# Optimization experiments

Hardware: AMD Instinct MI355X
Metric: run time of the kernel (lower is better)

Reference implementation:

```python
import jax, jax.numpy as jnp
import numpy as np

B, S, D = 4, 2048, 1024
E, F = 8, 4096


def setup_inputs() -> dict:
    key = jax.random.key(0)
    ks = jax.random.split(key, 5)
    x = jax.random.normal(ks[0], (B, S, D), dtype=jnp.float32)
    switch_w = jax.random.normal(ks[1], (D, E), dtype=jnp.float32) * (D ** -0.5)
    switch_b = jnp.zeros((E,), dtype=jnp.float32)
    w1 = jax.random.normal(ks[2], (E, D, F), dtype=jnp.float32) * (D ** -0.5)
    b1 = jnp.zeros((E, F), dtype=jnp.float32)
    w2 = jax.random.normal(ks[3], (E, F, D), dtype=jnp.float32) * (F ** -0.5)
    b2 = jnp.zeros((E, D), dtype=jnp.float32)
    return {"x": x, "switch_w": switch_w, "switch_b": switch_b,
            "w1": w1, "b1": b1, "w2": w2, "b2": b2}


def reference(x, switch_w, switch_b, w1, b1, w2, b2):
    b, s, d = x.shape
    t = x.reshape(-1, d)                                  # [T, D] tokens
    logits = t @ switch_w + switch_b                      # [T, E]
    route_prob = jax.nn.softmax(logits, axis=-1)
    route_prob_max = jnp.max(route_prob, axis=-1)         # [T]
    routes = jnp.argmax(route_prob, axis=-1)              # [T] top-1 expert

    out = jnp.zeros_like(t)
    n_experts = w1.shape[0]
    for e in range(n_experts):                            # small fixed expert loop
        h = jax.nn.gelu(t @ w1[e] + b1[e])                # [T, F]
        y = h @ w2[e] + b2[e]                             # [T, D]
        mask = (routes == e)[:, None]
        out = jnp.where(mask, y, out)                     # scatter-combine by route

    out = out * route_prob_max[:, None]                   # is_scale_prob=True
    return out.reshape(b, s, d)
```

## Files before the change

kernel.cpp:

```cpp
#include <hip/hip_runtime.h>
#include <hip/hip_bf16.h>
#include <math.h>

#define T_TOK 8192
#define DIM   1024
#define NEXP  8
#define FF    4096
#define BM    256
#define BN    256
#define BK    64
#define TPAD  (T_TOK + NEXP * BM)
#define NCBLK 32
#define MT    (TPAD / BM)
#define NG1   640
#define NG2   160
#define NT2   4096

typedef __attribute__((ext_vector_type(4))) float  f32x4;
typedef __attribute__((ext_vector_type(8))) __bf16 bf16x8;

__global__ __launch_bounds__(256) void router_kernel(const float* __restrict__ x,
                              const float* __restrict__ sw, const float* __restrict__ sb,
                              int* __restrict__ route, float* __restrict__ scale,
                              __hip_bfloat16* __restrict__ xb)
{
    int wave = threadIdx.x >> 6, lane = threadIdx.x & 63;
    int t = blockIdx.x * 4 + wave;
    const float* xr = x + (size_t)t * DIM + lane * 16;

    float xv[16];
#pragma unroll
    for (int i = 0; i < 4; ++i)
        *(float4*)&xv[i * 4] = *(const float4*)(xr + i * 4);

    bf16x8 u0, u1;
#pragma unroll
    for (int i = 0; i < 8; ++i) { u0[i] = (__bf16)xv[i]; u1[i] = (__bf16)xv[i + 8]; }
    __hip_bfloat16* xo = xb + (size_t)t * DIM + lane * 16;
    *(bf16x8*)xo = u0;
    *(bf16x8*)(xo + 8) = u1;

    double acc[NEXP];
#pragma unroll
    for (int e = 0; e < NEXP; ++e) acc[e] = 0.0;
    const float* swp = sw + lane * 16 * NEXP;
#pragma unroll
    for (int j = 0; j < 16; ++j) {
        float4 s0 = *(const float4*)(swp + j * 8);
        float4 s1 = *(const float4*)(swp + j * 8 + 4);
        double xd = (double)xv[j];
        acc[0] += xd * (double)s0.x; acc[1] += xd * (double)s0.y;
        acc[2] += xd * (double)s0.z; acc[3] += xd * (double)s0.w;
        acc[4] += xd * (double)s1.x; acc[5] += xd * (double)s1.y;
        acc[6] += xd * (double)s1.z; acc[7] += xd * (double)s1.w;
    }
#pragma unroll
    for (int e = 0; e < NEXP; ++e) {
        double v = acc[e];
        for (int off = 32; off; off >>= 1) v += __shfl_down(v, off);
        acc[e] = v;
    }
    if (lane == 0) {
        double m = -1e300; int am = 0;
#pragma unroll
        for (int e = 0; e < NEXP; ++e) {
            double v = acc[e] + (double)sb[e];
            acc[e] = v;
            if (v > m) { m = v; am = e; }
        }
        double s = 0.0;
#pragma unroll
        for (int e = 0; e < NEXP; ++e) s += exp(acc[e] - m);
        route[t] = am;
        scale[t] = (float)(1.0 / s);
    }
}

__global__ __launch_bounds__(256) void count_kernel(const int* __restrict__ route,
                                                    int* __restrict__ bc)
{
    __shared__ int c[NEXP];
    if (threadIdx.x < NEXP) c[threadIdx.x] = 0;
    __syncthreads();
    int t = blockIdx.x * 256 + threadIdx.x;
    atomicAdd(&c[route[t]], 1);
    __syncthreads();
    if (threadIdx.x < NEXP) bc[blockIdx.x * NEXP + threadIdx.x] = c[threadIdx.x];
}

__global__ __launch_bounds__(64) void offsets_kernel(const int* __restrict__ bc,
                                                     int* __restrict__ offPad,
                                                     int* __restrict__ base)
{
    int l = threadIdx.x & 31;
    int cnt[NEXP], pre[NEXP], tot[NEXP];
#pragma unroll
    for (int e = 0; e < NEXP; ++e) cnt[e] = bc[l * NEXP + e];
#pragma unroll
    for (int e = 0; e < NEXP; ++e) {
        int v = cnt[e];
#pragma unroll
        for (int d = 1; d < 32; d <<= 1) {
            int u = __shfl_up(v, d, 32);
            if (l >= d) v += u;
        }
        pre[e] = v - cnt[e];
        tot[e] = __shfl(v, 31, 32);
    }
    int o = 0, off[NEXP];
#pragma unroll
    for (int e = 0; e < NEXP; ++e) {
        off[e] = o;
        o += ((tot[e] + BM - 1) / BM) * BM;
    }
    if (l == 0) {
#pragma unroll
        for (int e = 0; e < NEXP; ++e) offPad[e] = off[e];
        offPad[NEXP] = o;
    }
#pragma unroll
    for (int e = 0; e < NEXP; ++e) base[l * NEXP + e] = off[e] + pre[e];
}

__global__ __launch_bounds__(256) void scatter_kernel(const int* __restrict__ route,
                                                      const int* __restrict__ base,
                                                      int* __restrict__ perm)
{
    __shared__ int cur[NEXP];
    if (threadIdx.x < NEXP) cur[threadIdx.x] = base[blockIdx.x * NEXP + threadIdx.x];
    __syncthreads();
    int t = blockIdx.x * 256 + threadIdx.x;
    int pos = atomicAdd(&cur[route[t]], 1);
    perm[pos] = t;
}

__global__ __launch_bounds__(256) void transpose_cvt64(const float* __restrict__ src,
                                                       __hip_bfloat16* __restrict__ dst,
                                                       int R, int C)
{
    __shared__ float tile[64][65];
    size_t bofs = (size_t)blockIdx.z * (size_t)R * (size_t)C;
    int c0 = blockIdx.x * 64, r0 = blockIdx.y * 64;
    int t = threadIdx.x;
    int tx = t & 15, ty = t >> 4;
#pragma unroll
    for (int i = 0; i < 4; ++i) {
        int r = ty + i * 16;
        float4 v = *(const float4*)(src + bofs + (size_t)(r0 + r) * C + c0 + tx * 4);
        tile[r][tx * 4 + 0] = v.x; tile[r][tx * 4 + 1] = v.y;
        tile[r][tx * 4 + 2] = v.z; tile[r][tx * 4 + 3] = v.w;
    }
    __syncthreads();
    int sx = t & 7, sy = t >> 3;
#pragma unroll
    for (int i = 0; i < 2; ++i) {
        int oc = sy + i * 32;
        bf16x8 u;
#pragma unroll
        for (int j = 0; j < 8; ++j)
            u[j] = (__bf16)tile[sx * 8 + j][oc];
        *(bf16x8*)(dst + bofs + (size_t)(c0 + oc) * R + r0 + sx * 8) = u;
    }
}

#define STAGE_A(b, h, t) do { \
    __builtin_amdgcn_global_load_lds((const __attribute__((address_space(1))) void*)(aSrc[h][0] + (size_t)(t) * 64), \
        (__attribute__((address_space(3))) void*)(ldsA + (b) * 32768 + (h) * 16384 + wid * 1024), 16, 0, 0); \
    __builtin_amdgcn_global_load_lds((const __attribute__((address_space(1))) void*)(aSrc[h][1] + (size_t)(t) * 64), \
        (__attribute__((address_space(3))) void*)(ldsA + (b) * 32768 + (h) * 16384 + (wid + 8) * 1024), 16, 0, 0); \
} while (0)

#define STAGE_B(b, h, t) do { \
    __builtin_amdgcn_global_load_lds((const __attribute__((address_space(1))) void*)(bSrc[h][0] + (size_t)(t) * 64), \
        (__attribute__((address_space(3))) void*)(ldsB + (b) * 32768 + (h) * 16384 + wid * 1024), 16, 0, 0); \
    __builtin_amdgcn_global_load_lds((const __attribute__((address_space(1))) void*)(bSrc[h][1] + (size_t)(t) * 64), \
        (__attribute__((address_space(3))) void*)(ldsB + (b) * 32768 + (h) * 16384 + (wid + 8) * 1024), 16, 0, 0); \
} while (0)

#define VMW asm volatile("s_waitcnt vmcnt(4)" ::: "memory")

#define PHASE(B_, MH, KS, LOADB, STAGEX, VMX) do { \
    __builtin_amdgcn_sched_barrier(0); \
    bf16x8 af[4]; \
    _Pragma("unroll") \
    for (int i_ = 0; i_ < 4; ++i_) \
        af[i_] = *(const bf16x8*)(aRd + (B_) * 32768 + ((MH) * 4 + i_) * 2048 + kOff[KS]); \
    if (LOADB) { \
        _Pragma("unroll") \
        for (int n_ = 0; n_ < 4; ++n_) \
            bfr[KS][n_] = *(const bf16x8*)(bRd + (B_) * 32768 + n_ * 2048 + kOff[KS]); \
    } \
    STAGEX; \
    __builtin_amdgcn_s_barrier(); \
    asm volatile("s_waitcnt lgkmcnt(0)" ::: "memory"); \
    __builtin_amdgcn_sched_barrier(0); \
    __builtin_amdgcn_s_setprio(1); \
    _Pragma("unroll") \
    for (int i_ = 0; i_ < 4; ++i_) \
        _Pragma("unroll") \
        for (int n_ = 0; n_ < 4; ++n_) \
            acc[(MH) * 4 + i_][n_] = __builtin_amdgcn_mfma_f32_16x16x32_bf16(af[i_], bfr[KS][n_], acc[(MH) * 4 + i_][n_], 0, 0, 0); \
    __builtin_amdgcn_s_setprio(0); \
    VMX; \
    __builtin_amdgcn_s_barrier(); \
} while (0)

template<int MODE>
__global__ __launch_bounds__(512, 2) void moe_gemm8(
    const __hip_bfloat16* __restrict__ A,
    const __hip_bfloat16* __restrict__ Bw,
    const float* __restrict__ bias,
    const int* __restrict__ offPad,
    const int* __restrict__ perm,
    const float* __restrict__ scale,
    __hip_bfloat16* __restrict__ Hout,
    float* __restrict__ Out,
    const float* __restrict__ w2src,
    __hip_bfloat16* __restrict__ w2tdst,
    const int K, const int N)
{
    __shared__ char lds[131072];
    const int tid = threadIdx.x;
    const int bid = blockIdx.x;
    const int NG  = MODE ? NG2 : NG1;

    if (MODE == 0 && bid >= NG1) {
        const int j    = bid - NG1;
        const int t2   = tid & 255;
        const int half = tid >> 8;
        const int tile_id = j * 2 + half;
        const int cx = tile_id & 15;
        const int ry = (tile_id >> 4) & 63;
        const int ez = tile_id >> 10;
        float (*tl)[65] = (float (*)[65])(lds + half * 17408);
        const float* src = w2src + (size_t)ez * FF * DIM;
        __hip_bfloat16* dst = w2tdst + (size_t)ez * DIM * FF;
        const int c0 = cx * 64, r0 = ry * 64;
        const int tx = t2 & 15, ty = t2 >> 4;
#pragma unroll
        for (int i = 0; i < 4; ++i) {
            int r = ty + i * 16;
            float4 v = *(const float4*)(src + (size_t)(r0 + r) * DIM + c0 + tx * 4);
            tl[r][tx * 4 + 0] = v.x; tl[r][tx * 4 + 1] = v.y;
            tl[r][tx * 4 + 2] = v.z; tl[r][tx * 4 + 3] = v.w;
        }
        __syncthreads();
        const int sx = t2 & 7, sy = t2 >> 3;
#pragma unroll
        for (int i = 0; i < 2; ++i) {
            int oc = sy + i * 32;
            bf16x8 u;
#pragma unroll
            for (int jj = 0; jj < 8; ++jj)
                u[jj] = (__bf16)tl[sx * 8 + jj][oc];
            *(bf16x8*)(dst + (size_t)(c0 + oc) * FF + r0 + sx * 8) = u;
        }
        return;
    }

    const int swz = (bid & 7) * (NG >> 3) + (bid >> 3);
    const int mt  = swz % MT;
    const int nt  = swz / MT;
    const int m0  = mt * BM;
    if (m0 >= offPad[NEXP]) return;
    int e = 0;
    while (offPad[e + 1] <= m0) ++e;

    char* ldsA = lds;
    char* ldsB = lds + 65536;

    const int lane = tid & 63;
    const int wid  = tid >> 6;
    const int wr   = wid >> 2;
    const int wc   = wid & 3;
    const int g    = lane >> 4, rl = lane & 15;

    const __hip_bfloat16* Bp = Bw + (size_t)e * (size_t)N * (size_t)K;

    const int l3 = lane >> 3;
    const int colOff = ((lane & 7) ^ l3) * 8;
    const __hip_bfloat16* aSrc[2][2];
    const __hip_bfloat16* bSrc[2][2];
#pragma unroll
    for (int h = 0; h < 2; ++h)
#pragma unroll
        for (int j = 0; j < 2; ++j) {
            int r = (wid + j * 8) * 8 + l3;
            int arow = m0 + h * 128 + r;
            size_t ar;
            if (MODE == 0) { int tk = perm[arow]; ar = (size_t)(tk < 0 ? 0 : tk); }
            else           { ar = (size_t)arow; }
            aSrc[h][j] = A + ar * (size_t)K + colOff;
            bSrc[h][j] = Bp + (size_t)(nt * BN + h * 128 + r) * (size_t)K + colOff;
        }

    const char* aRd = ldsA + wr * 16384 + rl * 128;
    const char* bRd = ldsB + (wc >> 1) * 16384 + (wc & 1) * 8192 + rl * 128;
    int kOff[2];
    kOff[0] = ((0 * 4 + g) ^ (rl & 7)) * 16;
    kOff[1] = ((1 * 4 + g) ^ (rl & 7)) * 16;

    f32x4 acc[8][4];
#pragma unroll
    for (int i = 0; i < 8; ++i)
#pragma unroll
        for (int n = 0; n < 4; ++n) acc[i][n] = (f32x4)0.0f;
    bf16x8 bfr[2][4];

    const int ntiles = K >> 6;

    STAGE_A(0, 0, 0); STAGE_A(0, 1, 0);
    STAGE_B(0, 0, 0); STAGE_B(0, 1, 0);
    STAGE_B(1, 0, 1); STAGE_B(1, 1, 1);
    asm volatile("s_waitcnt vmcnt(4)" ::: "memory");
    __builtin_amdgcn_s_barrier();

    for (int it = 0; it < (ntiles >> 1); ++it) {
        const int t1 = 2 * it + 1;
        const int t2 = 2 * it + 2 < ntiles ? 2 * it + 2 : ntiles - 1;
        const int t3 = 2 * it + 3 < ntiles ? 2 * it + 3 : ntiles - 1;
        PHASE(0, 0, 0, true,  STAGE_A(1, 0, t1), );
        PHASE(0, 0, 1, true,  STAGE_A(1, 1, t1), );
        PHASE(0, 1, 0, false, STAGE_B(0, 0, t2), );
        PHASE(0, 1, 1, false, STAGE_B(0, 1, t2), VMW);
        PHASE(1, 0, 0, true,  STAGE_A(0, 0, t2), );
        PHASE(1, 0, 1, true,  STAGE_A(0, 1, t2), );
        PHASE(1, 1, 0, false, STAGE_B(1, 0, t3), );
        PHASE(1, 1, 1, false, STAGE_B(1, 1, t3), VMW);
    }
    asm volatile("s_waitcnt vmcnt(0)" ::: "memory");

    const int colBase = nt * BN + wc * 64;
    const int rowBase = m0 + wr * 128;
    float bcol[4];
#pragma unroll
    for (int n = 0; n < 4; ++n) bcol[n] = bias[(size_t)e * N + colBase + n * 16 + rl];

    if (MODE == 0) {
#pragma unroll
        for (int m = 0; m < 8; ++m) {
#pragma unroll
            for (int r = 0; r < 4; ++r) {
                int row = rowBase + m * 16 + g * 4 + r;
                __hip_bfloat16* hrow = Hout + (size_t)row * N + colBase;
#pragma unroll
                for (int n = 0; n < 4; ++n) {
                    float v = acc[m][n][r] + bcol[n];
                    float u = -1.5957691216057308f * (v + 0.044715f * v * v * v);
                    float gel = v / (1.f + __expf(u));
                    hrow[n * 16 + rl] = __float2bfloat16(gel);
                }
            }
        }
    } else {
#pragma unroll
        for (int m = 0; m < 8; ++m) {
#pragma unroll
            for (int r = 0; r < 4; ++r) {
                int row = rowBase + m * 16 + g * 4 + r;
                int tk = perm[row];
                if (tk >= 0) {
                    float sc = scale[tk];
                    float* orow = Out + (size_t)tk * N + colBase;
#pragma unroll
                    for (int n = 0; n < 4; ++n)
                        orow[n * 16 + rl] = (acc[m][n][r] + bcol[n]) * sc;
                }
            }
        }
    }
}

extern "C" void kernel_launch(void* const* d_in, const int* in_sizes, int n_in,
                              void* d_out, int out_size, void* d_ws, size_t ws_size,
                              hipStream_t stream)
{
    const float* x  = (const float*)d_in[0];
    const float* sw = (const float*)d_in[1];
    const float* sb = (const float*)d_in[2];
    const float* w1 = (const float*)d_in[3];
    const float* b1 = (const float*)d_in[4];
    const float* w2 = (const float*)d_in[5];
    const float* b2 = (const float*)d_in[6];
    float* out = (float*)d_out;
    char* ws = (char*)d_ws;

    int*   bc     = (int*)(ws + 1024);
    int*   base   = (int*)(ws + 2048);
    int*   offPad = (int*)(ws + 3072);
    int*   route  = (int*)(ws + 4096);
    float* scale  = (float*)(ws + 36864);
    int*   perm   = (int*)(ws + 69632);

    const size_t offXb   = 131072;
    const size_t szXb    = (size_t)T_TOK * DIM * 2;
    const size_t offW1   = offXb + szXb;
    const size_t szW     = (size_t)NEXP * DIM * FF * 2;
    const size_t offW2   = offW1 + szW;
    const size_t szH     = (size_t)TPAD * FF * 2;
    const size_t offHF   = offW2 + szW;
    const size_t needF   = offHF + szH;

    const bool fuseT = ws_size >= needF;

    __hip_bfloat16* xb  = (__hip_bfloat16*)(ws + offXb);
    __hip_bfloat16* w1t = (__hip_bfloat16*)(ws + offW1);
    __hip_bfloat16* w2t = (__hip_bfloat16*)(ws + (fuseT ? offW2 : offW1));
    __hip_bfloat16* h   = (__hip_bfloat16*)(ws + (fuseT ? offHF : offW2));

    hipMemsetAsync(perm, 0xFF, TPAD * 4, stream);

    router_kernel<<<T_TOK / 4, 256, 0, stream>>>(x, sw, sb, route, scale, xb);
    count_kernel<<<NCBLK, 256, 0, stream>>>(route, bc);
    offsets_kernel<<<1, 64, 0, stream>>>(bc, offPad, base);
    scatter_kernel<<<NCBLK, 256, 0, stream>>>(route, base, perm);

    transpose_cvt64<<<dim3(FF / 64, DIM / 64, NEXP), 256, 0, stream>>>(w1, w1t, DIM, FF);

    if (fuseT) {
        moe_gemm8<0><<<NG1 + NT2, 512, 0, stream>>>(
            xb, w1t, b1, offPad, perm, scale, h, nullptr, w2, w2t, DIM, FF);
        moe_gemm8<1><<<NG2, 512, 0, stream>>>(
            h, w2t, b2, offPad, perm, scale, nullptr, out, nullptr, nullptr, FF, DIM);
    } else {
        moe_gemm8<0><<<NG1, 512, 0, stream>>>(
            xb, w1t, b1, offPad, perm, scale, h, nullptr, nullptr, nullptr, DIM, FF);
        transpose_cvt64<<<dim3(DIM / 64, FF / 64, NEXP), 256, 0, stream>>>(w2, w2t, FF, DIM);
        moe_gemm8<1><<<NG2, 512, 0, stream>>>(
            h, w2t, b2, offPad, perm, scale, nullptr, out, nullptr, nullptr, FF, DIM);
    }
}
```

Before: 315.6 us.

## Shrink MoE GEMM tiles to 128x256 with BK=32 triple-buffered pipeline

```diff
diff --git a/kernel.cpp b/kernel.cpp
--- a/kernel.cpp
+++ b/kernel.cpp
@@ -6,14 +6,13 @@
 #define DIM   1024
 #define NEXP  8
 #define FF    4096
-#define BM    256
+#define BM    128
 #define BN    256
-#define BK    64
 #define TPAD  (T_TOK + NEXP * BM)
 #define NCBLK 32
 #define MT    (TPAD / BM)
-#define NG1   640
-#define NG2   160
+#define NG1   (16 * MT)
+#define NG2   (4 * MT)
 #define NT2   4096
 
 typedef __attribute__((ext_vector_type(4))) float  f32x4;
@@ -163,50 +162,44 @@
     }
 }
 
-#define STAGE_A(b, h, t) do { \
-    __builtin_amdgcn_global_load_lds((const __attribute__((address_space(1))) void*)(aSrc[h][0] + (size_t)(t) * 64), \
-        (__attribute__((address_space(3))) void*)(ldsA + (b) * 32768 + (h) * 16384 + wid * 1024), 16, 0, 0); \
-    __builtin_amdgcn_global_load_lds((const __attribute__((address_space(1))) void*)(aSrc[h][1] + (size_t)(t) * 64), \
-        (__attribute__((address_space(3))) void*)(ldsA + (b) * 32768 + (h) * 16384 + (wid + 8) * 1024), 16, 0, 0); \
+#define GL2LDS(g, l) __builtin_amdgcn_global_load_lds( \
+    (const __attribute__((address_space(1))) void*)(g), \
+    (__attribute__((address_space(3))) void*)(l), 16, 0, 0)
+
+#define STG(TS, BUFS) do { \
+    const int ts_ = (TS) < NT ? (TS) : NT - 1; \
+    const size_t ko_ = (size_t)ts_ * 32; \
+    GL2LDS(aSrc + ko_, lds + (BUFS) * 24576 + dstA); \
+    GL2LDS(bSrc0 + ko_, lds + (BUFS) * 24576 + 8192 + dstA); \
+    GL2LDS(bSrc1 + ko_, lds + (BUFS) * 24576 + 16384 + dstA); \
 } while (0)
 
-#define STAGE_B(b, h, t) do { \
-    __builtin_amdgcn_global_load_lds((const __attribute__((address_space(1))) void*)(bSrc[h][0] + (size_t)(t) * 64), \
-        (__attribute__((address_space(3))) void*)(ldsB + (b) * 32768 + (h) * 16384 + wid * 1024), 16, 0, 0); \
-    __builtin_amdgcn_global_load_lds((const __attribute__((address_space(1))) void*)(bSrc[h][1] + (size_t)(t) * 64), \
-        (__attribute__((address_space(3))) void*)(ldsB + (b) * 32768 + (h) * 16384 + (wid + 8) * 1024), 16, 0, 0); \
-} while (0)
-
-#define VMW asm volatile("s_waitcnt vmcnt(4)" ::: "memory")
-
-#define PHASE(B_, MH, KS, LOADB, STAGEX, VMX) do { \
+#define PH(BUFR, TS, BUFS) do { \
     __builtin_amdgcn_sched_barrier(0); \
-    bf16x8 af[4]; \
+    bf16x8 af[4], bf[4]; \
     _Pragma("unroll") \
     for (int i_ = 0; i_ < 4; ++i_) \
-        af[i_] = *(const bf16x8*)(aRd + (B_) * 32768 + ((MH) * 4 + i_) * 2048 + kOff[KS]); \
-    if (LOADB) { \
-        _Pragma("unroll") \
-        for (int n_ = 0; n_ < 4; ++n_) \
-            bfr[KS][n_] = *(const bf16x8*)(bRd + (B_) * 32768 + n_ * 2048 + kOff[KS]); \
-    } \
-    STAGEX; \
+        af[i_] = *(const bf16x8*)(lds + (BUFR) * 24576 + aOff + i_ * 1024); \
+    _Pragma("unroll") \
+    for (int n_ = 0; n_ < 4; ++n_) \
+        bf[n_] = *(const bf16x8*)(lds + (BUFR) * 24576 + bOff + n_ * 1024); \
+    STG(TS, BUFS); \
     __builtin_amdgcn_s_barrier(); \
     asm volatile("s_waitcnt lgkmcnt(0)" ::: "memory"); \
     __builtin_amdgcn_sched_barrier(0); \
     __builtin_amdgcn_s_setprio(1); \
     _Pragma("unroll") \
-    for (int i_ = 0; i_ < 4; ++i_) \
+    for (int m_ = 0; m_ < 4; ++m_) \
         _Pragma("unroll") \
         for (int n_ = 0; n_ < 4; ++n_) \
-            acc[(MH) * 4 + i_][n_] = __builtin_amdgcn_mfma_f32_16x16x32_bf16(af[i_], bfr[KS][n_], acc[(MH) * 4 + i_][n_], 0, 0, 0); \
+            acc[m_][n_] = __builtin_amdgcn_mfma_f32_16x16x32_bf16(af[m_], bf[n_], acc[m_][n_], 0, 0, 0); \
     __builtin_amdgcn_s_setprio(0); \
-    VMX; \
+    asm volatile("s_waitcnt vmcnt(3)" ::: "memory"); \
     __builtin_amdgcn_s_barrier(); \
 } while (0)
 
 template<int MODE>
-__global__ __launch_bounds__(512, 2) void moe_gemm8(
+__global__ __launch_bounds__(512, 4) void moe_gemm32(
     const __hip_bfloat16* __restrict__ A,
     const __hip_bfloat16* __restrict__ Bw,
     const float* __restrict__ bias,
@@ -216,13 +209,16 @@
     __hip_bfloat16* __restrict__ Hout,
     float* __restrict__ Out,
     const float* __restrict__ w2src,
-    __hip_bfloat16* __restrict__ w2tdst,
-    const int K, const int N)
-{
-    __shared__ char lds[131072];
+    __hip_bfloat16* __restrict__ w2tdst)
+{
+    constexpr int K  = MODE ? FF : DIM;
+    constexpr int N  = MODE ? DIM : FF;
+    constexpr int NT = K / 32;
+    constexpr int NG = MODE ? NG2 : NG1;
+
+    __shared__ char lds[73728];
     const int tid = threadIdx.x;
     const int bid = blockIdx.x;
-    const int NG  = MODE ? NG2 : NG1;
 
     if (MODE == 0 && bid >= NG1) {
         const int j    = bid - NG1;
@@ -266,9 +262,6 @@
     int e = 0;
     while (offPad[e + 1] <= m0) ++e;
 
-    char* ldsA = lds;
-    char* ldsB = lds + 65536;
-
     const int lane = tid & 63;
     const int wid  = tid >> 6;
     const int wr   = wid >> 2;
@@ -277,68 +270,50 @@
 
     const __hip_bfloat16* Bp = Bw + (size_t)e * (size_t)N * (size_t)K;
 
-    const int l3 = lane >> 3;
-    const int colOff = ((lane & 7) ^ l3) * 8;
-    const __hip_bfloat16* aSrc[2][2];
-    const __hip_bfloat16* bSrc[2][2];
-#pragma unroll
-    for (int h = 0; h < 2; ++h)
-#pragma unroll
-        for (int j = 0; j < 2; ++j) {
-            int r = (wid + j * 8) * 8 + l3;
-            int arow = m0 + h * 128 + r;
-            size_t ar;
-            if (MODE == 0) { int tk = perm[arow]; ar = (size_t)(tk < 0 ? 0 : tk); }
-            else           { ar = (size_t)arow; }
-            aSrc[h][j] = A + ar * (size_t)K + colOff;
-            bSrc[h][j] = Bp + (size_t)(nt * BN + h * 128 + r) * (size_t)K + colOff;
-        }
-
-    const char* aRd = ldsA + wr * 16384 + rl * 128;
-    const char* bRd = ldsB + (wc >> 1) * 16384 + (wc & 1) * 8192 + rl * 128;
-    int kOff[2];
-    kOff[0] = ((0 * 4 + g) ^ (rl & 7)) * 16;
-    kOff[1] = ((1 * 4 + g) ^ (rl & 7)) * 16;
-
-    f32x4 acc[8][4];
-#pragma unroll
-    for (int i = 0; i < 8; ++i)
+    const int colElem = (((lane & 3) ^ ((lane >> 2) & 3) ^ ((lane >> 4) & 1))) * 8;
+    const int srow = wid * 16 + (lane >> 2);
+    size_t ar;
+    if (MODE == 0) { int tk = perm[m0 + srow]; ar = (size_t)(tk < 0 ? 0 : tk); }
+    else           { ar = (size_t)(m0 + srow); }
+    const __hip_bfloat16* aSrc  = A  + ar * (size_t)K + colElem;
+    const __hip_bfloat16* bSrc0 = Bp + (size_t)(nt * BN + srow) * (size_t)K + colElem;
+    const __hip_bfloat16* bSrc1 = bSrc0 + (size_t)128 * K;
+    const int dstA = wid * 1024 + lane * 16;
+
+    const int kOff = ((g ^ (rl & 3) ^ ((rl >> 2) & 1))) * 16;
+    const int aOff = wr * 4096 + rl * 64 + kOff;
+    const int bOff = 8192 + wc * 4096 + rl * 64 + kOff;
+
+    f32x4 acc[4][4];
+#pragma unroll
+    for (int i = 0; i < 4; ++i)
 #pragma unroll
         for (int n = 0; n < 4; ++n) acc[i][n] = (f32x4)0.0f;
-    bf16x8 bfr[2][4];
-
-    const int ntiles = K >> 6;
-
-    STAGE_A(0, 0, 0); STAGE_A(0, 1, 0);
-    STAGE_B(0, 0, 0); STAGE_B(0, 1, 0);
-    STAGE_B(1, 0, 1); STAGE_B(1, 1, 1);
-    asm volatile("s_waitcnt vmcnt(4)" ::: "memory");
+
+    STG(0, 0); STG(1, 1);
+    asm volatile("s_waitcnt vmcnt(3)" ::: "memory");
     __builtin_amdgcn_s_barrier();
 
-    for (int it = 0; it < (ntiles >> 1); ++it) {
-        const int t1 = 2 * it + 1;
-        const int t2 = 2 * it + 2 < ntiles ? 2 * it + 2 : ntiles - 1;
-        const int t3 = 2 * it + 3 < ntiles ? 2 * it + 3 : ntiles - 1;
-        PHASE(0, 0, 0, true,  STAGE_A(1, 0, t1), );
-        PHASE(0, 0, 1, true,  STAGE_A(1, 1, t1), );
-        PHASE(0, 1, 0, false, STAGE_B(0, 0, t2), );
-        PHASE(0, 1, 1, false, STAGE_B(0, 1, t2), VMW);
-        PHASE(1, 0, 0, true,  STAGE_A(0, 0, t2), );
-        PHASE(1, 0, 1, true,  STAGE_A(0, 1, t2), );
-        PHASE(1, 1, 0, false, STAGE_B(1, 0, t3), );
-        PHASE(1, 1, 1, false, STAGE_B(1, 1, t3), VMW);
-    }
+#pragma unroll 1
+    for (int tb = 0; tb < NT / 3; ++tb) {
+        const int t = tb * 3;
+        PH(0, t + 2, 2);
+        PH(1, t + 3, 0);
+        PH(2, t + 4, 1);
+    }
+    PH(0, NT, 2);
+    PH(1, NT + 1, 0);
     asm volatile("s_waitcnt vmcnt(0)" ::: "memory");
 
     const int colBase = nt * BN + wc * 64;
-    const int rowBase = m0 + wr * 128;
+    const int rowBase = m0 + wr * 64;
     float bcol[4];
 #pragma unroll
     for (int n = 0; n < 4; ++n) bcol[n] = bias[(size_t)e * N + colBase + n * 16 + rl];
 
     if (MODE == 0) {
 #pragma unroll
-        for (int m = 0; m < 8; ++m) {
+        for (int m = 0; m < 4; ++m) {
 #pragma unroll
             for (int r = 0; r < 4; ++r) {
                 int row = rowBase + m * 16 + g * 4 + r;
@@ -354,7 +329,7 @@
         }
     } else {
 #pragma unroll
-        for (int m = 0; m < 8; ++m) {
+        for (int m = 0; m < 4; ++m) {
 #pragma unroll
             for (int r = 0; r < 4; ++r) {
                 int row = rowBase + m * 16 + g * 4 + r;
@@ -392,14 +367,14 @@
     float* scale  = (float*)(ws + 36864);
     int*   perm   = (int*)(ws + 69632);
 
-    const size_t offXb   = 131072;
-    const size_t szXb    = (size_t)T_TOK * DIM * 2;
-    const size_t offW1   = offXb + szXb;
-    const size_t szW     = (size_t)NEXP * DIM * FF * 2;
-    const size_t offW2   = offW1 + szW;
-    const size_t szH     = (size_t)TPAD * FF * 2;
-    const size_t offHF   = offW2 + szW;
-    const size_t needF   = offHF + szH;
+    const size_t offXb = 131072;
+    const size_t szXb  = (size_t)T_TOK * DIM * 2;
+    const size_t offW1 = offXb + szXb;
+    const size_t szW   = (size_t)NEXP * DIM * FF * 2;
+    const size_t offW2 = offW1 + szW;
+    const size_t szH   = (size_t)TPAD * FF * 2;
+    const size_t offHF = offW2 + szW;
+    const size_t needF = offHF + szH;
 
     const bool fuseT = ws_size >= needF;
 
@@ -418,15 +393,15 @@
     transpose_cvt64<<<dim3(FF / 64, DIM / 64, NEXP), 256, 0, stream>>>(w1, w1t, DIM, FF);
 
     if (fuseT) {
-        moe_gemm8<0><<<NG1 + NT2, 512, 0, stream>>>(
-            xb, w1t, b1, offPad, perm, scale, h, nullptr, w2, w2t, DIM, FF);
-        moe_gemm8<1><<<NG2, 512, 0, stream>>>(
-            h, w2t, b2, offPad, perm, scale, nullptr, out, nullptr, nullptr, FF, DIM);
+        moe_gemm32<0><<<NG1 + NT2, 512, 0, stream>>>(
+            xb, w1t, b1, offPad, perm, scale, h, nullptr, w2, w2t);
+        moe_gemm32<1><<<NG2, 512, 0, stream>>>(
+            h, w2t, b2, offPad, perm, scale, nullptr, out, nullptr, nullptr);
     } else {
-        moe_gemm8<0><<<NG1, 512, 0, stream>>>(
-            xb, w1t, b1, offPad, perm, scale, h, nullptr, nullptr, nullptr, DIM, FF);
+        moe_gemm32<0><<<NG1, 512, 0, stream>>>(
+            xb, w1t, b1, offPad, perm, scale, h, nullptr, nullptr, nullptr);
         transpose_cvt64<<<dim3(DIM / 64, FF / 64, NEXP), 256, 0, stream>>>(w2, w2t, FF, DIM);
-        moe_gemm8<1><<<NG2, 512, 0, stream>>>(
-            h, w2t, b2, offPad, perm, scale, nullptr, out, nullptr, nullptr, FF, DIM);
-    }
-}
+        moe_gemm32<1><<<NG2, 512, 0, stream>>>(
+            h, w2t, b2, offPad, perm, scale, nullptr, out, nullptr, nullptr);
+    }
+}
```

After: 336.6 us. 1.07x slower.
